# Kernel optimization log

Hardware: AMD Instinct MI355X
Metric: run time of the kernel (lower is better)

Reference implementation:

```python
import jax, jax.numpy as jnp
import numpy as np

H = 8          # num_attention_heads
E = 768        # hidden_size
D = E // H     # attention_head_size = 96
LN_EPS = 1e-5


def setup_inputs() -> dict:
    key = jax.random.key(0)
    ks = jax.random.split(key, 12)
    B, S = 2, 2048
    inp = {
        "hidden_states": jax.random.normal(ks[0], (B, S, E), jnp.float32),
        "distance_matrix": jax.random.uniform(ks[1], (B, S, S), jnp.float32),
        "angle_matrix": jax.random.uniform(ks[2], (B, S, S), jnp.float32),
        "attention_mask": jnp.ones((B, S), jnp.float32),
        # Linear params, stored [in, out] so y = x @ W + b
        "Wq": jax.random.normal(ks[3], (E, E), jnp.float32) * 0.02,
        "bq": jnp.zeros((E,), jnp.float32),
        "Wk": jax.random.normal(ks[4], (E, E), jnp.float32) * 0.02,
        "bk": jnp.zeros((E,), jnp.float32),
        "Wv": jax.random.normal(ks[5], (E, E), jnp.float32) * 0.02,
        "bv": jnp.zeros((E,), jnp.float32),
        # distance_embedding / angle_embedding: Linear(1,1) -> scalar w,b
        "dist_w": jax.random.normal(ks[6], (), jnp.float32) * 0.5,
        "dist_b": jnp.zeros((), jnp.float32),
        "ang_w": jax.random.normal(ks[7], (), jnp.float32) * 0.5,
        "ang_b": jnp.zeros((), jnp.float32),
        "Wo": jax.random.normal(ks[8], (E, E), jnp.float32) * 0.02,
        "bo": jnp.zeros((E,), jnp.float32),
        "ln_gamma": jnp.ones((E,), jnp.float32),
        "ln_beta": jnp.zeros((E,), jnp.float32),
    }
    return inp


def _attention(hidden_states, distance_matrix, angle_matrix, attention_mask,
               Wq, bq, Wk, bk, Wv, bv, dist_w, dist_b, ang_w, ang_b,
               Wo, bo, ln_gamma, ln_beta):
    B, S, _ = hidden_states.shape
    # project and split heads -> [B, H, S, D]
    def heads(x):
        return x.reshape(B, S, H, D).transpose(0, 2, 1, 3)
    q = heads(hidden_states @ Wq + bq)
    k = heads(hidden_states @ Wk + bk)
    v = heads(hidden_states @ Wv + bv)

    scores = jnp.einsum("bhqd,bhkd->bhqk", q, k) / jnp.sqrt(jnp.float32(D))
    # fused pairwise biases, broadcast over heads
    bias = (dist_w * distance_matrix + dist_b) + (ang_w * angle_matrix + ang_b)
    scores = scores + bias[:, None, :, :]
    # additive mask: mask is [B, S] over key dim
    scores = scores + ((1.0 - attention_mask) * -10000.0)[:, None, None, :]

    probs = jax.nn.softmax(scores, axis=-1)  # dropout is identity at eval
    ctx = jnp.einsum("bhqk,bhkd->bhqd", probs, v)
    ctx = ctx.transpose(0, 2, 1, 3).reshape(B, S, E)

    out = ctx @ Wo + bo  # output dropout identity at eval
    res = out + hidden_states
    mu = jnp.mean(res, axis=-1, keepdims=True)
    var = jnp.var(res, axis=-1, keepdims=True)
    out = (res - mu) * jax.lax.rsqrt(var + LN_EPS) * ln_gamma + ln_beta
    return out, probs


def reference(hidden_states, distance_matrix, angle_matrix, attention_mask,
              Wq, bq, Wk, bk, Wv, bv, dist_w, dist_b, ang_w, ang_b,
              Wo, bo, ln_gamma, ln_beta):
    return _attention(hidden_states, distance_matrix, angle_matrix, attention_mask,
                      Wq, bq, Wk, bk, Wv, bv, dist_w, dist_b, ang_w, ang_b,
                      Wo, bo, ln_gamma, ln_beta)
```

## Files before the change

### kernel.cpp

```cpp
#include <hip/hip_runtime.h>
#include <math.h>

#define S_LEN 2048
#define BATCH 2
#define EMB 768
#define NH 8
#define HD 96
#define NTOK (BATCH*S_LEN)
#define RSQRT_D 0.10206207261596575f

typedef unsigned short u16;
typedef __attribute__((ext_vector_type(8))) short bf16x8;
typedef __attribute__((ext_vector_type(4))) float f32x4;

#define MFMA16(a,b,c) __builtin_amdgcn_mfma_f32_16x16x32_bf16(a,b,c,0,0,0)

__device__ __forceinline__ u16 f2bf(float f){
    unsigned u = __float_as_uint(f);
    return (u16)((u + 0x7fffu + ((u>>16)&1u)) >> 16);
}
__device__ __forceinline__ float bf2f(unsigned u){
    return __uint_as_float(u << 16);
}

union U16x8 { u16 u[8]; float4 f4; };
union U16x4 { u16 u[4]; uint2 v2; };

__global__ __launch_bounds__(256) void cvt_bf16_kernel(
    const float* __restrict__ src, u16* __restrict__ dst, int n4)
{
    int i = blockIdx.x * 256 + threadIdx.x;
    if (i < n4) {
        float4 v = ((const float4*)src)[i];
        U16x4 o;
        o.u[0] = f2bf(v.x); o.u[1] = f2bf(v.y); o.u[2] = f2bf(v.z); o.u[3] = f2bf(v.w);
        *(uint2*)(dst + (size_t)i*4) = o.v2;
    }
}

__global__ __launch_bounds__(256) void transcvt_kernel(
    const float* __restrict__ W, u16* __restrict__ Wt)
{
    __shared__ float T[64][65];
    const int t = threadIdx.x;
    const int k0 = blockIdx.y * 64, n0 = blockIdx.x * 64;
    #pragma unroll
    for (int i = 0; i < 4; ++i) {
        int idx = t + 256*i;
        int r = idx >> 4, c4 = idx & 15;
        float4 v = *(const float4*)(W + (size_t)(k0 + r)*EMB + n0 + c4*4);
        T[r][c4*4+0] = v.x; T[r][c4*4+1] = v.y; T[r][c4*4+2] = v.z; T[r][c4*4+3] = v.w;
    }
    __syncthreads();
    #pragma unroll
    for (int i = 0; i < 2; ++i) {
        int idx = t + 256*i;
        int n = idx >> 3, c = idx & 7;
        U16x8 o;
        #pragma unroll
        for (int e = 0; e < 8; ++e) o.u[e] = f2bf(T[c*8+e][n]);
        *(float4*)(Wt + (size_t)(n0 + n)*EMB + k0 + c*8) = o.f4;
    }
}

__global__ __launch_bounds__(256) void qkv_mfma_kernel(
    const u16* __restrict__ hsb,
    const u16* __restrict__ WqT, const float* __restrict__ bq,
    const u16* __restrict__ WkT, const float* __restrict__ bk,
    const u16* __restrict__ WvT, const float* __restrict__ bv,
    u16* __restrict__ qo, u16* __restrict__ ko, u16* __restrict__ vo)
{
    const u16* Wt; const float* bias; u16* out;
    if (blockIdx.z == 0)      { Wt = WqT; bias = bq; out = qo; }
    else if (blockIdx.z == 1) { Wt = WkT; bias = bk; out = ko; }
    else                      { Wt = WvT; bias = bv; out = vo; }

    __shared__ __align__(16) u16 As[64*64];
    __shared__ __align__(16) u16 Bs[64*64];
    const int tid = threadIdx.x;
    const int w = tid >> 6, lane = tid & 63, lh = lane & 15, g = lane >> 4;
    const int wm = w >> 1, wn = w & 1;
    const int row0 = blockIdx.y * 64, col0 = blockIdx.x * 64;

    f32x4 acc[2][2];
    #pragma unroll
    for (int i = 0; i < 2; ++i)
        #pragma unroll
        for (int j = 0; j < 2; ++j) acc[i][j] = (f32x4){0.f,0.f,0.f,0.f};

    for (int k0 = 0; k0 < EMB; k0 += 64) {
        __syncthreads();
        #pragma unroll
        for (int i = 0; i < 2; ++i) {
            int idx = tid + 256*i;
            int r = idx >> 3, c = idx & 7;
            float4 a4 = *(const float4*)(hsb + (size_t)(row0 + r)*EMB + k0 + c*8);
            *(float4*)(As + ((size_t)r*8 + (c ^ (r & 7)))*8) = a4;
            float4 b4 = *(const float4*)(Wt + (size_t)(col0 + r)*EMB + k0 + c*8);
            *(float4*)(Bs + ((size_t)r*8 + (c ^ (r & 7)))*8) = b4;
        }
        __syncthreads();
        bf16x8 af[2][2], bfr[2][2];
        #pragma unroll
        for (int mt = 0; mt < 2; ++mt)
            #pragma unroll
            for (int kk = 0; kk < 2; ++kk) {
                int r = wm*32 + mt*16 + lh;
                af[mt][kk] = *(const bf16x8*)(As + ((size_t)r*8 + ((kk*4+g) ^ (lh & 7)))*8);
            }
        #pragma unroll
        for (int nt = 0; nt < 2; ++nt)
            #pragma unroll
            for (int kk = 0; kk < 2; ++kk) {
                int r = wn*32 + nt*16 + lh;
                bfr[nt][kk] = *(const bf16x8*)(Bs + ((size_t)r*8 + ((kk*4+g) ^ (lh & 7)))*8);
            }
        #pragma unroll
        for (int mt = 0; mt < 2; ++mt)
            #pragma unroll
            for (int nt = 0; nt < 2; ++nt)
                #pragma unroll
                for (int kk = 0; kk < 2; ++kk)
                    acc[mt][nt] = MFMA16(af[mt][kk], bfr[nt][kk], acc[mt][nt]);
    }

    #pragma unroll
    for (int mt = 0; mt < 2; ++mt)
        #pragma unroll
        for (int nt = 0; nt < 2; ++nt)
            #pragma unroll
            for (int r = 0; r < 4; ++r) {
                int tt = row0 + wm*32 + mt*16 + g*4 + r;
                int o  = col0 + wn*32 + nt*16 + lh;
                float val = acc[mt][nt][r] + bias[o];
                int b = tt >> 11, s = tt & (S_LEN - 1);
                int h = o / HD, d = o - h*HD;
                out[((size_t)(b*NH + h)*S_LEN + s)*HD + d] = f2bf(val);
            }
}

__global__ __launch_bounds__(256) void vtrans_kernel(
    const u16* __restrict__ vb, u16* __restrict__ vt)
{
    const int bh = blockIdx.y;
    const int s0 = blockIdx.x * 64;
    __shared__ __align__(16) u16 T[64*96];
    const int t = threadIdx.x;
    #pragma unroll
    for (int i = 0; i < 3; ++i) {
        int idx = t + 256*i;
        int s = idx / 12, c = idx % 12;
        float4 v = *(const float4*)(vb + ((size_t)bh*S_LEN + s0 + s)*HD + c*8);
        *(float4*)(T + ((size_t)s*12 + c)*8) = v;
    }
    __syncthreads();
    #pragma unroll
    for (int i = 0; i < 3; ++i) {
        int idx = t + 256*i;
        int d = idx >> 3, c = idx & 7;
        U16x8 o;
        #pragma unroll
        for (int e = 0; e < 8; ++e) o.u[e] = T[(size_t)(c*8+e)*HD + d];
        *(float4*)(vt + ((size_t)bh*HD + d)*S_LEN + s0 + c*8) = o.f4;
    }
}

__global__ __launch_bounds__(512) void fused_attn_kernel(
    const u16* __restrict__ qbf, const u16* __restrict__ kbf,
    const u16* __restrict__ vt,
    const float* __restrict__ dist, const float* __restrict__ ang,
    const float* __restrict__ mask,
    const float* __restrict__ pdw, const float* __restrict__ pdb,
    const float* __restrict__ paw, const float* __restrict__ pab,
    float* __restrict__ probs, u16* __restrict__ ctxb)
{
    const int bh = blockIdx.y, b = bh >> 3, h = bh & 7;
    const int q0 = blockIdx.x * 32;
    const int tid = threadIdx.x;
    const int lane = tid & 63, w = tid >> 6, lh = lane & 15, g = lane >> 4;
    const int rt = w >> 2;
    const int ct = w & 3;

    __shared__ __align__(16) u16 Us[32*2048];
    __shared__ __align__(16) u16 Ks[64*96];
    __shared__ __align__(16) float Sf[32*68];
    __shared__ float mL[32];

    const int kr_s = tid / 12, kc_s = tid - (tid / 12) * 12;
    const int kr2_s = (tid + 512) / 12, kc2_s = (tid + 512) - ((tid + 512) / 12) * 12;
    const int vr_s = tid >> 3, vc_s = tid & 7;
    const int vr2_s = (tid + 512) >> 3, vc2_s = (tid + 512) & 7;

    u16* Qtmp = (u16*)Sf;
    if (tid < 384) {
        int r = tid / 12, c = tid % 12;
        float4 v = *(const float4*)(qbf + ((size_t)bh*S_LEN + q0 + r)*HD + c*8);
        *(float4*)(Qtmp + ((size_t)r*12 + (c ^ ((r >> 1) & 3)))*8) = v;
    }
    {
        float4 v = *(const float4*)(kbf + ((size_t)bh*S_LEN + kr_s)*HD + kc_s*8);
        *(float4*)(Ks + ((size_t)kr_s*12 + (kc_s ^ ((kr_s >> 1) & 3)))*8) = v;
        if (tid < 256) {
            float4 v2 = *(const float4*)(kbf + ((size_t)bh*S_LEN + kr2_s)*HD + kc2_s*8);
            *(float4*)(Ks + ((size_t)kr2_s*12 + (kc2_s ^ ((kr2_s >> 1) & 3)))*8) = v2;
        }
    }
    __syncthreads();
    bf16x8 qf[3];
    #pragma unroll
    for (int kk = 0; kk < 3; ++kk) {
        int r = rt*16 + lh;
        qf[kk] = *(const bf16x8*)(Qtmp + ((size_t)r*12 + ((kk*4+g) ^ ((r >> 1) & 3)))*8);
    }
    __syncthreads();

    const float DW = *pdw, AW = *paw, CB = *pdb + *pab;
    const int trow = tid >> 4;
    const int c4   = tid & 15;
    const size_t drow = ((size_t)b*S_LEN + q0 + trow)*S_LEN;
    const int uoff = (trow*8 + ((c4 >> 1) ^ (trow & 7)))*8 + (c4 & 1)*4;

    float lpart = 0.f;

    for (int kt = 0; kt < 32; ++kt) {
        int coff = kt*64 + c4*4;
        float4 kreg0, kreg1;
        if (kt < 31) {
            kreg0 = *(const float4*)(kbf + ((size_t)bh*S_LEN + (kt+1)*64 + kr_s)*HD + kc_s*8);
            if (tid < 256)
                kreg1 = *(const float4*)(kbf + ((size_t)bh*S_LEN + (kt+1)*64 + kr2_s)*HD + kc2_s*8);
        }
        float4 d4 = *(const float4*)(dist + drow + coff);
        float4 g4 = *(const float4*)(ang  + drow + coff);
        float4 m4 = *(const float4*)(mask + b*S_LEN + coff);

        __builtin_amdgcn_s_setprio(1);
        f32x4 acc = (f32x4){0.f,0.f,0.f,0.f};
        #pragma unroll
        for (int kk = 0; kk < 3; ++kk) {
            int kr = ct*16 + lh;
            bf16x8 kf = *(const bf16x8*)(Ks + ((size_t)kr*12 + ((kk*4+g) ^ ((kr >> 1) & 3)))*8);
            acc = MFMA16(qf[kk], kf, acc);
        }
        __builtin_amdgcn_s_setprio(0);
        #pragma unroll
        for (int r = 0; r < 4; ++r)
            Sf[(rt*16 + g*4 + r)*68 + ct*16 + lh] = acc[r];
        __syncthreads();

        float4 s4 = *(const float4*)&Sf[trow*68 + c4*4];
        float e0 = __expf(s4.x*RSQRT_D + DW*d4.x + AW*g4.x + CB + (1.f - m4.x) * -10000.f);
        float e1 = __expf(s4.y*RSQRT_D + DW*d4.y + AW*g4.y + CB + (1.f - m4.y) * -10000.f);
        float e2 = __expf(s4.z*RSQRT_D + DW*d4.z + AW*g4.z + CB + (1.f - m4.z) * -10000.f);
        float e3 = __expf(s4.w*RSQRT_D + DW*d4.w + AW*g4.w + CB + (1.f - m4.w) * -10000.f);
        lpart += (e0 + e1) + (e2 + e3);
        U16x4 uk;
        uk.u[0] = f2bf(e0); uk.u[1] = f2bf(e1); uk.u[2] = f2bf(e2); uk.u[3] = f2bf(e3);
        *(uint2*)(Us + (size_t)kt*2048 + uoff) = uk.v2;

        if (kt < 31) {
            *(float4*)(Ks + ((size_t)kr_s*12 + (kc_s ^ ((kr_s >> 1) & 3)))*8) = kreg0;
            if (tid < 256)
                *(float4*)(Ks + ((size_t)kr2_s*12 + (kc2_s ^ ((kr2_s >> 1) & 3)))*8) = kreg1;
        }
        __syncthreads();
    }

    #pragma unroll
    for (int off = 1; off <= 8; off <<= 1) lpart += __shfl_xor(lpart, off);
    if (c4 == 0) mL[trow] = 1.0f / lpart;
    {
        float4 v4 = *(const float4*)(vt + ((size_t)bh*HD + vr_s)*S_LEN + vc_s*8);
        *(float4*)(Ks + ((size_t)vr_s*8 + (vc_s ^ (vr_s & 7)))*8) = v4;
        if (tid < 256) {
            float4 v42 = *(const float4*)(vt + ((size_t)bh*HD + vr2_s)*S_LEN + vc2_s*8);
            *(float4*)(Ks + ((size_t)vr2_s*8 + (vc2_s ^ (vr2_s & 7)))*8) = v42;
        }
    }
    __syncthreads();

    const float invl_row = mL[trow];
    const int dt1 = ct;
    const bool two = (ct < 2);
    const int dt2 = ct + 4;
    f32x4 accA = (f32x4){0.f,0.f,0.f,0.f};
    f32x4 accB = (f32x4){0.f,0.f,0.f,0.f};

    for (int kt = 0; kt < 32; ++kt) {
        float4 vreg0, vreg1;
        if (kt < 31) {
            vreg0 = *(const float4*)(vt + ((size_t)bh*HD + vr_s)*S_LEN + (kt+1)*64 + vc_s*8);
            if (tid < 256)
                vreg1 = *(const float4*)(vt + ((size_t)bh*HD + vr2_s)*S_LEN + (kt+1)*64 + vc2_s*8);
        }
        {
            uint2 uu = *(const uint2*)(Us + (size_t)kt*2048 + uoff);
            float4 p;
            p.x = bf2f(uu.x & 0xffffu)*invl_row; p.y = bf2f(uu.x >> 16)*invl_row;
            p.z = bf2f(uu.y & 0xffffu)*invl_row; p.w = bf2f(uu.y >> 16)*invl_row;
            *(float4*)(probs + ((size_t)bh*S_LEN + q0 + trow)*S_LEN + kt*64 + c4*4) = p;
        }
        int prow = rt*16 + lh;
        bf16x8 pa[2];
        #pragma unroll
        for (int kk = 0; kk < 2; ++kk)
            pa[kk] = *(const bf16x8*)(Us + (size_t)kt*2048 + ((size_t)prow*8 + ((kk*4+g) ^ (prow & 7)))*8);
        __builtin_amdgcn_s_setprio(1);
        #pragma unroll
        for (int kk = 0; kk < 2; ++kk) {
            int vr = dt1*16 + lh;
            bf16x8 vf = *(const bf16x8*)(Ks + ((size_t)vr*8 + ((kk*4+g) ^ (vr & 7)))*8);
            accA = MFMA16(pa[kk], vf, accA);
        }
        if (two) {
            #pragma unroll
            for (int kk = 0; kk < 2; ++kk) {
                int vr = dt2*16 + lh;
                bf16x8 vf = *(const bf16x8*)(Ks + ((size_t)vr*8 + ((kk*4+g) ^ (vr & 7)))*8);
                accB = MFMA16(pa[kk], vf, accB);
            }
        }
        __builtin_amdgcn_s_setprio(0);
        __syncthreads();
        if (kt < 31) {
            *(float4*)(Ks + ((size_t)vr_s*8 + (vc_s ^ (vr_s & 7)))*8) = vreg0;
            if (tid < 256)
                *(float4*)(Ks + ((size_t)vr2_s*8 + (vc2_s ^ (vr2_s & 7)))*8) = vreg1;
        }
        __syncthreads();
    }

    float ils[4];
    #pragma unroll
    for (int r = 0; r < 4; ++r) ils[r] = mL[rt*16 + g*4 + r];
    #pragma unroll
    for (int r = 0; r < 4; ++r) {
        int qrow = q0 + rt*16 + g*4 + r;
        ctxb[((size_t)(b*S_LEN + qrow))*EMB + h*HD + dt1*16 + lh] = f2bf(accA[r] * ils[r]);
        if (two)
            ctxb[((size_t)(b*S_LEN + qrow))*EMB + h*HD + dt2*16 + lh] = f2bf(accB[r] * ils[r]);
    }
}

__global__ __launch_bounds__(256) void out_mfma_kernel(
    const u16* __restrict__ ctxb, const u16* __restrict__ WoT,
    const float* __restrict__ bo, const float* __restrict__ hs,
    float* __restrict__ res)
{
    __shared__ __align__(16) u16 As[64*64];
    __shared__ __align__(16) u16 Bs[64*64];
    const int tid = threadIdx.x;
    const int w = tid >> 6, lane = tid & 63, lh = lane & 15, g = lane >> 4;
    const int wm = w >> 1, wn = w & 1;
    const int row0 = blockIdx.y * 64, col0 = blockIdx.x * 64;

    f32x4 acc[2][2];
    #pragma unroll
    for (int i = 0; i < 2; ++i)
        #pragma unroll
        for (int j = 0; j < 2; ++j) acc[i][j] = (f32x4){0.f,0.f,0.f,0.f};

    for (int k0 = 0; k0 < EMB; k0 += 64) {
        __syncthreads();
        #pragma unroll
        for (int i = 0; i < 2; ++i) {
            int idx = tid + 256*i;
            int r = idx >> 3, c = idx & 7;
            float4 a4 = *(const float4*)(ctxb + (size_t)(row0 + r)*EMB + k0 + c*8);
            *(float4*)(As + ((size_t)r*8 + (c ^ (r & 7)))*8) = a4;
            float4 b4 = *(const float4*)(WoT + (size_t)(col0 + r)*EMB + k0 + c*8);
            *(float4*)(Bs + ((size_t)r*8 + (c ^ (r & 7)))*8) = b4;
        }
        __syncthreads();
        bf16x8 af[2][2], bfr[2][2];
        #pragma unroll
        for (int mt = 0; mt < 2; ++mt)
            #pragma unroll
            for (int kk = 0; kk < 2; ++kk) {
                int r = wm*32 + mt*16 + lh;
                af[mt][kk] = *(const bf16x8*)(As + ((size_t)r*8 + ((kk*4+g) ^ (lh & 7)))*8);
            }
        #pragma unroll
        for (int nt = 0; nt < 2; ++nt)
            #pragma unroll
            for (int kk = 0; kk < 2; ++kk) {
                int r = wn*32 + nt*16 + lh;
                bfr[nt][kk] = *(const bf16x8*)(Bs + ((size_t)r*8 + ((kk*4+g) ^ (lh & 7)))*8);
            }
        #pragma unroll
        for (int mt = 0; mt < 2; ++mt)
            #pragma unroll
            for (int nt = 0; nt < 2; ++nt)
                #pragma unroll
                for (int kk = 0; kk < 2; ++kk)
                    acc[mt][nt] = MFMA16(af[mt][kk], bfr[nt][kk], acc[mt][nt]);
    }

    #pragma unroll
    for (int mt = 0; mt < 2; ++mt)
        #pragma unroll
        for (int nt = 0; nt < 2; ++nt)
            #pragma unroll
            for (int r = 0; r < 4; ++r) {
                int tt = row0 + wm*32 + mt*16 + g*4 + r;
                int o  = col0 + wn*32 + nt*16 + lh;
                res[(size_t)tt*EMB + o] = acc[mt][nt][r] + bo[o] + hs[(size_t)tt*EMB + o];
            }
}

__device__ __forceinline__ float block_sum256(float v, float* red) {
    #pragma unroll
    for (int off = 32; off > 0; off >>= 1) v += __shfl_down(v, off);
    int lane = threadIdx.x & 63, w = threadIdx.x >> 6;
    __syncthreads();
    if (lane == 0) red[w] = v;
    __syncthreads();
    return red[0] + red[1] + red[2] + red[3];
}

__global__ __launch_bounds__(256) void ln_kernel(
    float* __restrict__ res, const float* __restrict__ gamma, const float* __restrict__ beta)
{
    const int t = blockIdx.x;
    float* row = res + (size_t)t * EMB;
    const int tid = threadIdx.x;
    __shared__ float red[4];

    float x0 = row[tid], x1 = row[tid + 256], x2 = row[tid + 512];
    float s = block_sum256(x0 + x1 + x2, red);
    float mu = s * (1.0f / (float)EMB);
    float d0 = x0 - mu, d1 = x1 - mu, d2 = x2 - mu;
    float sq = block_sum256(d0*d0 + d1*d1 + d2*d2, red);
    float var = sq * (1.0f / (float)EMB);
    float scale = rsqrtf(var + 1e-5f);

    row[tid]       = d0 * scale * gamma[tid]       + beta[tid];
    row[tid + 256] = d1 * scale * gamma[tid + 256] + beta[tid + 256];
    row[tid + 512] = d2 * scale * gamma[tid + 512] + beta[tid + 512];
}

extern "C" void kernel_launch(void* const* d_in, const int* in_sizes, int n_in,
                              void* d_out, int out_size, void* d_ws, size_t ws_size,
                              hipStream_t stream)
{
    (void)in_sizes; (void)n_in; (void)out_size; (void)ws_size;

    const float* hs   = (const float*)d_in[0];
    const float* dist = (const float*)d_in[1];
    const float* ang  = (const float*)d_in[2];
    const float* mask = (const float*)d_in[3];
    const float* Wq = (const float*)d_in[4];  const float* bq = (const float*)d_in[5];
    const float* Wk = (const float*)d_in[6];  const float* bk = (const float*)d_in[7];
    const float* Wv = (const float*)d_in[8];  const float* bv = (const float*)d_in[9];
    const float* dw = (const float*)d_in[10]; const float* db = (const float*)d_in[11];
    const float* aw = (const float*)d_in[12]; const float* ab = (const float*)d_in[13];
    const float* Wo = (const float*)d_in[14]; const float* bo = (const float*)d_in[15];
    const float* gamma = (const float*)d_in[16]; const float* beta = (const float*)d_in[17];

    float* out   = (float*)d_out;
    float* probs = out + (size_t)NTOK * EMB;

    u16* hsb = (u16*)d_ws;
    u16* WqT = hsb + (size_t)NTOK*EMB;
    u16* WkT = WqT + (size_t)EMB*EMB;
    u16* WvT = WkT + (size_t)EMB*EMB;
    u16* WoT = WvT + (size_t)EMB*EMB;
    u16* qb  = WoT + (size_t)EMB*EMB;
    u16* kb  = qb + (size_t)NTOK*EMB;
    u16* vb  = kb + (size_t)NTOK*EMB;
    u16* vtb = vb + (size_t)NTOK*EMB;
    u16* ctxb = qb;

    cvt_bf16_kernel<<<dim3(NTOK*EMB/4/256), dim3(256), 0, stream>>>(hs, hsb, NTOK*EMB/4);
    transcvt_kernel<<<dim3(12,12), dim3(256), 0, stream>>>(Wq, WqT);
    transcvt_kernel<<<dim3(12,12), dim3(256), 0, stream>>>(Wk, WkT);
    transcvt_kernel<<<dim3(12,12), dim3(256), 0, stream>>>(Wv, WvT);
    transcvt_kernel<<<dim3(12,12), dim3(256), 0, stream>>>(Wo, WoT);

    qkv_mfma_kernel<<<dim3(EMB/64, NTOK/64, 3), dim3(256), 0, stream>>>(
        hsb, WqT, bq, WkT, bk, WvT, bv, qb, kb, vb);

    vtrans_kernel<<<dim3(S_LEN/64, BATCH*NH), dim3(256), 0, stream>>>(vb, vtb);

    fused_attn_kernel<<<dim3(S_LEN/32, BATCH*NH), dim3(512), 0, stream>>>(
        qb, kb, vtb, dist, ang, mask, dw, db, aw, ab, probs, ctxb);

    out_mfma_kernel<<<dim3(EMB/64, NTOK/64), dim3(256), 0, stream>>>(
        ctxb, WoT, bo, hs, out);

    ln_kernel<<<dim3(NTOK), dim3(256), 0, stream>>>(out, gamma, beta);
}
```

Baseline: 260.1 us.

## Deepen K/V and bias prefetch to two tiles ahead in attention loops

Unrolls the QK-softmax and PV loops by two and keeps two register sets of K/V tile loads in flight, issued two tiles ahead of use. The distance, angle and mask loads are also issued one tile early, so global-memory latency is better hidden behind the MFMA and exp work. In the QK loop the K shared-memory store now happens right after the MFMA sync instead of after the epilogue. This costs extra registers, which may reduce occupancy.

```diff
diff --git a/kernel.cpp b/kernel.cpp
--- a/kernel.cpp
+++ b/kernel.cpp
@@ -191,6 +191,12 @@
     const int vr_s = tid >> 3, vc_s = tid & 7;
     const int vr2_s = (tid + 512) >> 3, vc2_s = (tid + 512) & 7;
 
+    const float DW = *pdw, AW = *paw, CB = *pdb + *pab;
+    const int trow = tid >> 4;
+    const int c4   = tid & 15;
+    const size_t drow = ((size_t)b*S_LEN + q0 + trow)*S_LEN;
+    const int uoff = (trow*8 + ((c4 >> 1) ^ (trow & 7)))*8 + (c4 & 1)*4;
+
     u16* Qtmp = (u16*)Sf;
     if (tid < 384) {
         int r = tid / 12, c = tid % 12;
@@ -205,6 +211,17 @@
             *(float4*)(Ks + ((size_t)kr2_s*12 + (kc2_s ^ ((kr2_s >> 1) & 3)))*8) = v2;
         }
     }
+    float4 kA0, kA1, kB0, kB1;
+    kA0 = *(const float4*)(kbf + ((size_t)bh*S_LEN + 1*64 + kr_s)*HD + kc_s*8);
+    if (tid < 256)
+        kA1 = *(const float4*)(kbf + ((size_t)bh*S_LEN + 1*64 + kr2_s)*HD + kc2_s*8);
+    kB0 = *(const float4*)(kbf + ((size_t)bh*S_LEN + 2*64 + kr_s)*HD + kc_s*8);
+    if (tid < 256)
+        kB1 = *(const float4*)(kbf + ((size_t)bh*S_LEN + 2*64 + kr2_s)*HD + kc2_s*8);
+    float4 dc4 = *(const float4*)(dist + drow + c4*4);
+    float4 gc4 = *(const float4*)(ang  + drow + c4*4);
+    float4 mc4 = *(const float4*)(mask + b*S_LEN + c4*4);
+
     __syncthreads();
     bf16x8 qf[3];
     #pragma unroll
@@ -214,26 +231,10 @@
     }
     __syncthreads();
 
-    const float DW = *pdw, AW = *paw, CB = *pdb + *pab;
-    const int trow = tid >> 4;
-    const int c4   = tid & 15;
-    const size_t drow = ((size_t)b*S_LEN + q0 + trow)*S_LEN;
-    const int uoff = (trow*8 + ((c4 >> 1) ^ (trow & 7)))*8 + (c4 & 1)*4;
-
     float lpart = 0.f;
-
-    for (int kt = 0; kt < 32; ++kt) {
-        int coff = kt*64 + c4*4;
-        float4 kreg0, kreg1;
-        if (kt < 31) {
-            kreg0 = *(const float4*)(kbf + ((size_t)bh*S_LEN + (kt+1)*64 + kr_s)*HD + kc_s*8);
-            if (tid < 256)
-                kreg1 = *(const float4*)(kbf + ((size_t)bh*S_LEN + (kt+1)*64 + kr2_s)*HD + kc2_s*8);
-        }
-        float4 d4 = *(const float4*)(dist + drow + coff);
-        float4 g4 = *(const float4*)(ang  + drow + coff);
-        float4 m4 = *(const float4*)(mask + b*S_LEN + coff);
-
+    float4 dN4, gN4, mN4;
+
+    auto qkmfma = [&]() {
         __builtin_amdgcn_s_setprio(1);
         f32x4 acc = (f32x4){0.f,0.f,0.f,0.f};
         #pragma unroll
@@ -246,8 +247,8 @@
         #pragma unroll
         for (int r = 0; r < 4; ++r)
             Sf[(rt*16 + g*4 + r)*68 + ct*16 + lh] = acc[r];
-        __syncthreads();
-
+    };
+    auto epiA = [&](int kt, const float4& d4, const float4& g4, const float4& m4) {
         float4 s4 = *(const float4*)&Sf[trow*68 + c4*4];
         float e0 = __expf(s4.x*RSQRT_D + DW*d4.x + AW*g4.x + CB + (1.f - m4.x) * -10000.f);
         float e1 = __expf(s4.y*RSQRT_D + DW*d4.y + AW*g4.y + CB + (1.f - m4.y) * -10000.f);
@@ -257,12 +258,49 @@
         U16x4 uk;
         uk.u[0] = f2bf(e0); uk.u[1] = f2bf(e1); uk.u[2] = f2bf(e2); uk.u[3] = f2bf(e3);
         *(uint2*)(Us + (size_t)kt*2048 + uoff) = uk.v2;
-
-        if (kt < 31) {
-            *(float4*)(Ks + ((size_t)kr_s*12 + (kc_s ^ ((kr_s >> 1) & 3)))*8) = kreg0;
-            if (tid < 256)
-                *(float4*)(Ks + ((size_t)kr2_s*12 + (kc2_s ^ ((kr2_s >> 1) & 3)))*8) = kreg1;
-        }
+    };
+
+    for (int kt = 0; kt < 32; kt += 2) {
+        qkmfma();
+        __syncthreads();
+        {
+            *(float4*)(Ks + ((size_t)kr_s*12 + (kc_s ^ ((kr_s >> 1) & 3)))*8) = kA0;
+            if (tid < 256)
+                *(float4*)(Ks + ((size_t)kr2_s*12 + (kc2_s ^ ((kr2_s >> 1) & 3)))*8) = kA1;
+        }
+        {
+            int coff = (kt+1)*64 + c4*4;
+            dN4 = *(const float4*)(dist + drow + coff);
+            gN4 = *(const float4*)(ang  + drow + coff);
+            mN4 = *(const float4*)(mask + b*S_LEN + coff);
+        }
+        if (kt + 3 < 32) {
+            kA0 = *(const float4*)(kbf + ((size_t)bh*S_LEN + (kt+3)*64 + kr_s)*HD + kc_s*8);
+            if (tid < 256)
+                kA1 = *(const float4*)(kbf + ((size_t)bh*S_LEN + (kt+3)*64 + kr2_s)*HD + kc2_s*8);
+        }
+        epiA(kt, dc4, gc4, mc4);
+        __syncthreads();
+
+        qkmfma();
+        __syncthreads();
+        if (kt + 2 < 32) {
+            *(float4*)(Ks + ((size_t)kr_s*12 + (kc_s ^ ((kr_s >> 1) & 3)))*8) = kB0;
+            if (tid < 256)
+                *(float4*)(Ks + ((size_t)kr2_s*12 + (kc2_s ^ ((kr2_s >> 1) & 3)))*8) = kB1;
+        }
+        if (kt + 2 < 32) {
+            int coff = (kt+2)*64 + c4*4;
+            dc4 = *(const float4*)(dist + drow + coff);
+            gc4 = *(const float4*)(ang  + drow + coff);
+            mc4 = *(const float4*)(mask + b*S_LEN + coff);
+        }
+        if (kt + 4 < 32) {
+            kB0 = *(const float4*)(kbf + ((size_t)bh*S_LEN + (kt+4)*64 + kr_s)*HD + kc_s*8);
+            if (tid < 256)
+                kB1 = *(const float4*)(kbf + ((size_t)bh*S_LEN + (kt+4)*64 + kr2_s)*HD + kc2_s*8);
+        }
+        epiA(kt+1, dN4, gN4, mN4);
         __syncthreads();
     }
 
@@ -277,6 +315,13 @@
             *(float4*)(Ks + ((size_t)vr2_s*8 + (vc2_s ^ (vr2_s & 7)))*8) = v42;
         }
     }
+    float4 vA0, vA1, vB0, vB1;
+    vA0 = *(const float4*)(vt + ((size_t)bh*HD + vr_s)*S_LEN + 1*64 + vc_s*8);
+    if (tid < 256)
+        vA1 = *(const float4*)(vt + ((size_t)bh*HD + vr2_s)*S_LEN + 1*64 + vc2_s*8);
+    vB0 = *(const float4*)(vt + ((size_t)bh*HD + vr_s)*S_LEN + 2*64 + vc_s*8);
+    if (tid < 256)
+        vB1 = *(const float4*)(vt + ((size_t)bh*HD + vr2_s)*S_LEN + 2*64 + vc2_s*8);
     __syncthreads();
 
     const float invl_row = mL[trow];
@@ -286,20 +331,12 @@
     f32x4 accA = (f32x4){0.f,0.f,0.f,0.f};
     f32x4 accB = (f32x4){0.f,0.f,0.f,0.f};
 
-    for (int kt = 0; kt < 32; ++kt) {
-        float4 vreg0, vreg1;
-        if (kt < 31) {
-            vreg0 = *(const float4*)(vt + ((size_t)bh*HD + vr_s)*S_LEN + (kt+1)*64 + vc_s*8);
-            if (tid < 256)
-                vreg1 = *(const float4*)(vt + ((size_t)bh*HD + vr2_s)*S_LEN + (kt+1)*64 + vc2_s*8);
-        }
-        {
-            uint2 uu = *(const uint2*)(Us + (size_t)kt*2048 + uoff);
-            float4 p;
-            p.x = bf2f(uu.x & 0xffffu)*invl_row; p.y = bf2f(uu.x >> 16)*invl_row;
-            p.z = bf2f(uu.y & 0xffffu)*invl_row; p.w = bf2f(uu.y >> 16)*invl_row;
-            *(float4*)(probs + ((size_t)bh*S_LEN + q0 + trow)*S_LEN + kt*64 + c4*4) = p;
-        }
+    auto pvstep = [&](int kt) {
+        uint2 uu = *(const uint2*)(Us + (size_t)kt*2048 + uoff);
+        float4 p;
+        p.x = bf2f(uu.x & 0xffffu)*invl_row; p.y = bf2f(uu.x >> 16)*invl_row;
+        p.z = bf2f(uu.y & 0xffffu)*invl_row; p.w = bf2f(uu.y >> 16)*invl_row;
+        *(float4*)(probs + ((size_t)bh*S_LEN + q0 + trow)*S_LEN + kt*64 + c4*4) = p;
         int prow = rt*16 + lh;
         bf16x8 pa[2];
         #pragma unroll
@@ -321,11 +358,34 @@
             }
         }
         __builtin_amdgcn_s_setprio(0);
-        __syncthreads();
-        if (kt < 31) {
-            *(float4*)(Ks + ((size_t)vr_s*8 + (vc_s ^ (vr_s & 7)))*8) = vreg0;
-            if (tid < 256)
-                *(float4*)(Ks + ((size_t)vr2_s*8 + (vc2_s ^ (vr2_s & 7)))*8) = vreg1;
+    };
+
+    for (int kt = 0; kt < 32; kt += 2) {
+        pvstep(kt);
+        __syncthreads();
+        {
+            *(float4*)(Ks + ((size_t)vr_s*8 + (vc_s ^ (vr_s & 7)))*8) = vA0;
+            if (tid < 256)
+                *(float4*)(Ks + ((size_t)vr2_s*8 + (vc2_s ^ (vr2_s & 7)))*8) = vA1;
+        }
+        if (kt + 3 < 32) {
+            vA0 = *(const float4*)(vt + ((size_t)bh*HD + vr_s)*S_LEN + (kt+3)*64 + vc_s*8);
+            if (tid < 256)
+                vA1 = *(const float4*)(vt + ((size_t)bh*HD + vr2_s)*S_LEN + (kt+3)*64 + vc2_s*8);
+        }
+        __syncthreads();
+
+        pvstep(kt+1);
+        __syncthreads();
+        if (kt + 2 < 32) {
+            *(float4*)(Ks + ((size_t)vr_s*8 + (vc_s ^ (vr_s & 7)))*8) = vB0;
+            if (tid < 256)
+                *(float4*)(Ks + ((size_t)vr2_s*8 + (vc2_s ^ (vr2_s & 7)))*8) = vB1;
+        }
+        if (kt + 4 < 32) {
+            vB0 = *(const float4*)(vt + ((size_t)bh*HD + vr_s)*S_LEN + (kt+4)*64 + vc_s*8);
+            if (tid < 256)
+                vB1 = *(const float4*)(vt + ((size_t)bh*HD + vr2_s)*S_LEN + (kt+4)*64 + vc2_s*8);
         }
         __syncthreads();
     }
```

Measured after the change: 264.1 us. No clear change (+1.6%).

## Split fused attention into row-sum pass and recompute-plus-PV pass

Applied to the files above, without the earlier changes.

Replaces the single fused attention kernel, which cached all exponentiated scores for a 32-row tile in 128KB of LDS, with two kernels. The first computes QK^T plus biases and writes only the per-row exp sums. The second recomputes the scores, normalizes and writes probs, then does PV through a small 64-column P buffer. This cuts LDS use per block to raise occupancy, but it doubles the QK^T work and the reads of the distance and angle matrices.

```diff
diff --git a/kernel.cpp b/kernel.cpp
--- a/kernel.cpp
+++ b/kernel.cpp
@@ -165,31 +165,26 @@
     }
 }
 
-__global__ __launch_bounds__(512) void fused_attn_kernel(
+__global__ __launch_bounds__(512) void scores_l_kernel(
     const u16* __restrict__ qbf, const u16* __restrict__ kbf,
-    const u16* __restrict__ vt,
     const float* __restrict__ dist, const float* __restrict__ ang,
     const float* __restrict__ mask,
     const float* __restrict__ pdw, const float* __restrict__ pdb,
     const float* __restrict__ paw, const float* __restrict__ pab,
-    float* __restrict__ probs, u16* __restrict__ ctxb)
-{
-    const int bh = blockIdx.y, b = bh >> 3, h = bh & 7;
+    float* __restrict__ lrow)
+{
+    const int bh = blockIdx.y, b = bh >> 3;
     const int q0 = blockIdx.x * 32;
     const int tid = threadIdx.x;
     const int lane = tid & 63, w = tid >> 6, lh = lane & 15, g = lane >> 4;
     const int rt = w >> 2;
     const int ct = w & 3;
 
-    __shared__ __align__(16) u16 Us[32*2048];
     __shared__ __align__(16) u16 Ks[64*96];
     __shared__ __align__(16) float Sf[32*68];
-    __shared__ float mL[32];
 
     const int kr_s = tid / 12, kc_s = tid - (tid / 12) * 12;
     const int kr2_s = (tid + 512) / 12, kc2_s = (tid + 512) - ((tid + 512) / 12) * 12;
-    const int vr_s = tid >> 3, vc_s = tid & 7;
-    const int vr2_s = (tid + 512) >> 3, vc2_s = (tid + 512) & 7;
 
     u16* Qtmp = (u16*)Sf;
     if (tid < 384) {
@@ -215,10 +210,8 @@
     __syncthreads();
 
     const float DW = *pdw, AW = *paw, CB = *pdb + *pab;
-    const int trow = tid >> 4;
-    const int c4   = tid & 15;
+    const int trow = tid >> 4, c4 = tid & 15;
     const size_t drow = ((size_t)b*S_LEN + q0 + trow)*S_LEN;
-    const int uoff = (trow*8 + ((c4 >> 1) ^ (trow & 7)))*8 + (c4 & 1)*4;
 
     float lpart = 0.f;
 
@@ -248,91 +241,176 @@
             Sf[(rt*16 + g*4 + r)*68 + ct*16 + lh] = acc[r];
         __syncthreads();
 
+        if (kt < 31) {
+            *(float4*)(Ks + ((size_t)kr_s*12 + (kc_s ^ ((kr_s >> 1) & 3)))*8) = kreg0;
+            if (tid < 256)
+                *(float4*)(Ks + ((size_t)kr2_s*12 + (kc2_s ^ ((kr2_s >> 1) & 3)))*8) = kreg1;
+        }
         float4 s4 = *(const float4*)&Sf[trow*68 + c4*4];
         float e0 = __expf(s4.x*RSQRT_D + DW*d4.x + AW*g4.x + CB + (1.f - m4.x) * -10000.f);
         float e1 = __expf(s4.y*RSQRT_D + DW*d4.y + AW*g4.y + CB + (1.f - m4.y) * -10000.f);
         float e2 = __expf(s4.z*RSQRT_D + DW*d4.z + AW*g4.z + CB + (1.f - m4.z) * -10000.f);
         float e3 = __expf(s4.w*RSQRT_D + DW*d4.w + AW*g4.w + CB + (1.f - m4.w) * -10000.f);
         lpart += (e0 + e1) + (e2 + e3);
-        U16x4 uk;
-        uk.u[0] = f2bf(e0); uk.u[1] = f2bf(e1); uk.u[2] = f2bf(e2); uk.u[3] = f2bf(e3);
-        *(uint2*)(Us + (size_t)kt*2048 + uoff) = uk.v2;
-
-        if (kt < 31) {
-            *(float4*)(Ks + ((size_t)kr_s*12 + (kc_s ^ ((kr_s >> 1) & 3)))*8) = kreg0;
-            if (tid < 256)
-                *(float4*)(Ks + ((size_t)kr2_s*12 + (kc2_s ^ ((kr2_s >> 1) & 3)))*8) = kreg1;
-        }
         __syncthreads();
     }
 
     #pragma unroll
     for (int off = 1; off <= 8; off <<= 1) lpart += __shfl_xor(lpart, off);
-    if (c4 == 0) mL[trow] = 1.0f / lpart;
+    if (c4 == 0) lrow[(bh << 11) + q0 + trow] = lpart;
+}
+
+__global__ __launch_bounds__(512) void attn_pv_kernel(
+    const u16* __restrict__ qbf, const u16* __restrict__ kbf,
+    const u16* __restrict__ vt,
+    const float* __restrict__ dist, const float* __restrict__ ang,
+    const float* __restrict__ mask,
+    const float* __restrict__ pdw, const float* __restrict__ pdb,
+    const float* __restrict__ paw, const float* __restrict__ pab,
+    const float* __restrict__ lrow,
+    float* __restrict__ probs, u16* __restrict__ ctxb)
+{
+    const int bh = blockIdx.y, b = bh >> 3, h = bh & 7;
+    const int q0 = blockIdx.x * 32;
+    const int tid = threadIdx.x;
+    const int lane = tid & 63, w = tid >> 6, lh = lane & 15, g = lane >> 4;
+    const int rt = w >> 2;
+    const int ct = w & 3;
+
+    __shared__ __align__(16) u16 Ks[64*96];
+    __shared__ __align__(16) u16 Vs[96*64];
+    __shared__ __align__(16) float Sf[32*68];
+    __shared__ __align__(16) u16 Ps[32*64];
+
+    const int kr_s = tid / 12, kc_s = tid - (tid / 12) * 12;
+    const int kr2_s = (tid + 512) / 12, kc2_s = (tid + 512) - ((tid + 512) / 12) * 12;
+    const int vr_s = tid >> 3, vc_s = tid & 7;
+    const int vr2_s = (tid + 512) >> 3, vc2_s = (tid + 512) & 7;
+
+    u16* Qtmp = (u16*)Sf;
+    if (tid < 384) {
+        int r = tid / 12, c = tid % 12;
+        float4 v = *(const float4*)(qbf + ((size_t)bh*S_LEN + q0 + r)*HD + c*8);
+        *(float4*)(Qtmp + ((size_t)r*12 + (c ^ ((r >> 1) & 3)))*8) = v;
+    }
     {
+        float4 v = *(const float4*)(kbf + ((size_t)bh*S_LEN + kr_s)*HD + kc_s*8);
+        *(float4*)(Ks + ((size_t)kr_s*12 + (kc_s ^ ((kr_s >> 1) & 3)))*8) = v;
+        if (tid < 256) {
+            float4 v2 = *(const float4*)(kbf + ((size_t)bh*S_LEN + kr2_s)*HD + kc2_s*8);
+            *(float4*)(Ks + ((size_t)kr2_s*12 + (kc2_s ^ ((kr2_s >> 1) & 3)))*8) = v2;
+        }
         float4 v4 = *(const float4*)(vt + ((size_t)bh*HD + vr_s)*S_LEN + vc_s*8);
-        *(float4*)(Ks + ((size_t)vr_s*8 + (vc_s ^ (vr_s & 7)))*8) = v4;
+        *(float4*)(Vs + ((size_t)vr_s*8 + (vc_s ^ (vr_s & 7)))*8) = v4;
         if (tid < 256) {
             float4 v42 = *(const float4*)(vt + ((size_t)bh*HD + vr2_s)*S_LEN + vc2_s*8);
-            *(float4*)(Ks + ((size_t)vr2_s*8 + (vc2_s ^ (vr2_s & 7)))*8) = v42;
-        }
-    }
-    __syncthreads();
-
-    const float invl_row = mL[trow];
+            *(float4*)(Vs + ((size_t)vr2_s*8 + (vc2_s ^ (vr2_s & 7)))*8) = v42;
+        }
+    }
+    __syncthreads();
+    bf16x8 qf[3];
+    #pragma unroll
+    for (int kk = 0; kk < 3; ++kk) {
+        int r = rt*16 + lh;
+        qf[kk] = *(const bf16x8*)(Qtmp + ((size_t)r*12 + ((kk*4+g) ^ ((r >> 1) & 3)))*8);
+    }
+    __syncthreads();
+
+    const float DW = *pdw, AW = *paw, CB = *pdb + *pab;
+    const int trow = tid >> 4, c4 = tid & 15;
+    const size_t drow = ((size_t)b*S_LEN + q0 + trow)*S_LEN;
+    const int uoffP = (trow*8 + ((c4 >> 1) ^ (trow & 7)))*8 + (c4 & 1)*4;
+    const float invl_row = 1.0f / lrow[(bh << 11) + q0 + trow];
+
     const int dt1 = ct;
     const bool two = (ct < 2);
     const int dt2 = ct + 4;
+    const int prowPV = rt*16 + lh;
     f32x4 accA = (f32x4){0.f,0.f,0.f,0.f};
     f32x4 accB = (f32x4){0.f,0.f,0.f,0.f};
 
     for (int kt = 0; kt < 32; ++kt) {
-        float4 vreg0, vreg1;
+        int coff = kt*64 + c4*4;
+        float4 kp0, kp1, vp0, vp1;
         if (kt < 31) {
-            vreg0 = *(const float4*)(vt + ((size_t)bh*HD + vr_s)*S_LEN + (kt+1)*64 + vc_s*8);
+            kp0 = *(const float4*)(kbf + ((size_t)bh*S_LEN + (kt+1)*64 + kr_s)*HD + kc_s*8);
             if (tid < 256)
-                vreg1 = *(const float4*)(vt + ((size_t)bh*HD + vr2_s)*S_LEN + (kt+1)*64 + vc2_s*8);
+                kp1 = *(const float4*)(kbf + ((size_t)bh*S_LEN + (kt+1)*64 + kr2_s)*HD + kc2_s*8);
+            vp0 = *(const float4*)(vt + ((size_t)bh*HD + vr_s)*S_LEN + (kt+1)*64 + vc_s*8);
+            if (tid < 256)
+                vp1 = *(const float4*)(vt + ((size_t)bh*HD + vr2_s)*S_LEN + (kt+1)*64 + vc2_s*8);
+        }
+        float4 d4 = *(const float4*)(dist + drow + coff);
+        float4 g4 = *(const float4*)(ang  + drow + coff);
+        float4 m4 = *(const float4*)(mask + b*S_LEN + coff);
+
+        __builtin_amdgcn_s_setprio(1);
+        f32x4 acc = (f32x4){0.f,0.f,0.f,0.f};
+        #pragma unroll
+        for (int kk = 0; kk < 3; ++kk) {
+            int kr = ct*16 + lh;
+            bf16x8 kf = *(const bf16x8*)(Ks + ((size_t)kr*12 + ((kk*4+g) ^ ((kr >> 1) & 3)))*8);
+            acc = MFMA16(qf[kk], kf, acc);
+        }
+        __builtin_amdgcn_s_setprio(0);
+        #pragma unroll
+        for (int r = 0; r < 4; ++r)
+            Sf[(rt*16 + g*4 + r)*68 + ct*16 + lh] = acc[r];
+        __syncthreads();
+
+        if (kt < 31) {
+            *(float4*)(Ks + ((size_t)kr_s*12 + (kc_s ^ ((kr_s >> 1) & 3)))*8) = kp0;
+            if (tid < 256)
+                *(float4*)(Ks + ((size_t)kr2_s*12 + (kc2_s ^ ((kr2_s >> 1) & 3)))*8) = kp1;
         }
         {
-            uint2 uu = *(const uint2*)(Us + (size_t)kt*2048 + uoff);
+            float4 s4 = *(const float4*)&Sf[trow*68 + c4*4];
+            float e0 = __expf(s4.x*RSQRT_D + DW*d4.x + AW*g4.x + CB + (1.f - m4.x) * -10000.f);
+            float e1 = __expf(s4.y*RSQRT_D + DW*d4.y + AW*g4.y + CB + (1.f - m4.y) * -10000.f);
+            float e2 = __expf(s4.z*RSQRT_D + DW*d4.z + AW*g4.z + CB + (1.f - m4.z) * -10000.f);
+            float e3 = __expf(s4.w*RSQRT_D + DW*d4.w + AW*g4.w + CB + (1.f - m4.w) * -10000.f);
             float4 p;
-            p.x = bf2f(uu.x & 0xffffu)*invl_row; p.y = bf2f(uu.x >> 16)*invl_row;
-            p.z = bf2f(uu.y & 0xffffu)*invl_row; p.w = bf2f(uu.y >> 16)*invl_row;
-            *(float4*)(probs + ((size_t)bh*S_LEN + q0 + trow)*S_LEN + kt*64 + c4*4) = p;
-        }
-        int prow = rt*16 + lh;
+            p.x = e0*invl_row; p.y = e1*invl_row; p.z = e2*invl_row; p.w = e3*invl_row;
+            *(float4*)(probs + ((size_t)bh*S_LEN + q0 + trow)*S_LEN + coff) = p;
+            U16x4 uk;
+            uk.u[0] = f2bf(e0); uk.u[1] = f2bf(e1); uk.u[2] = f2bf(e2); uk.u[3] = f2bf(e3);
+            *(uint2*)(Ps + uoffP) = uk.v2;
+        }
+        __syncthreads();
+
         bf16x8 pa[2];
         #pragma unroll
         for (int kk = 0; kk < 2; ++kk)
-            pa[kk] = *(const bf16x8*)(Us + (size_t)kt*2048 + ((size_t)prow*8 + ((kk*4+g) ^ (prow & 7)))*8);
+            pa[kk] = *(const bf16x8*)(Ps + ((size_t)prowPV*8 + ((kk*4+g) ^ (prowPV & 7)))*8);
         __builtin_amdgcn_s_setprio(1);
         #pragma unroll
         for (int kk = 0; kk < 2; ++kk) {
             int vr = dt1*16 + lh;
-            bf16x8 vf = *(const bf16x8*)(Ks + ((size_t)vr*8 + ((kk*4+g) ^ (vr & 7)))*8);
+            bf16x8 vf = *(const bf16x8*)(Vs + ((size_t)vr*8 + ((kk*4+g) ^ (vr & 7)))*8);
             accA = MFMA16(pa[kk], vf, accA);
         }
         if (two) {
             #pragma unroll
             for (int kk = 0; kk < 2; ++kk) {
                 int vr = dt2*16 + lh;
-                bf16x8 vf = *(const bf16x8*)(Ks + ((size_t)vr*8 + ((kk*4+g) ^ (vr & 7)))*8);
+                bf16x8 vf = *(const bf16x8*)(Vs + ((size_t)vr*8 + ((kk*4+g) ^ (vr & 7)))*8);
                 accB = MFMA16(pa[kk], vf, accB);
             }
         }
         __builtin_amdgcn_s_setprio(0);
         __syncthreads();
+
         if (kt < 31) {
-            *(float4*)(Ks + ((size_t)vr_s*8 + (vc_s ^ (vr_s & 7)))*8) = vreg0;
+            *(float4*)(Vs + ((size_t)vr_s*8 + (vc_s ^ (vr_s & 7)))*8) = vp0;
             if (tid < 256)
-                *(float4*)(Ks + ((size_t)vr2_s*8 + (vc2_s ^ (vr2_s & 7)))*8) = vreg1;
-        }
-        __syncthreads();
+                *(float4*)(Vs + ((size_t)vr2_s*8 + (vc2_s ^ (vr2_s & 7)))*8) = vp1;
+        }
     }
 
     float ils[4];
     #pragma unroll
-    for (int r = 0; r < 4; ++r) ils[r] = mL[rt*16 + g*4 + r];
+    for (int r = 0; r < 4; ++r)
+        ils[r] = 1.0f / lrow[(bh << 11) + q0 + rt*16 + g*4 + r];
     #pragma unroll
     for (int r = 0; r < 4; ++r) {
         int qrow = q0 + rt*16 + g*4 + r;
@@ -470,6 +548,7 @@
     u16* vb  = kb + (size_t)NTOK*EMB;
     u16* vtb = vb + (size_t)NTOK*EMB;
     u16* ctxb = qb;
+    float* lrow = (float*)(vtb + (size_t)NTOK*EMB);
 
     cvt_bf16_kernel<<<dim3(NTOK*EMB/4/256), dim3(256), 0, stream>>>(hs, hsb, NTOK*EMB/4);
     transcvt_kernel<<<dim3(12,12), dim3(256), 0, stream>>>(Wq, WqT);
@@ -482,8 +561,11 @@
 
     vtrans_kernel<<<dim3(S_LEN/64, BATCH*NH), dim3(256), 0, stream>>>(vb, vtb);
 
-    fused_attn_kernel<<<dim3(S_LEN/32, BATCH*NH), dim3(512), 0, stream>>>(
-        qb, kb, vtb, dist, ang, mask, dw, db, aw, ab, probs, ctxb);
+    scores_l_kernel<<<dim3(S_LEN/32, BATCH*NH), dim3(512), 0, stream>>>(
+        qb, kb, dist, ang, mask, dw, db, aw, ab, lrow);
+
+    attn_pv_kernel<<<dim3(S_LEN/32, BATCH*NH), dim3(512), 0, stream>>>(
+        qb, kb, vtb, dist, ang, mask, dw, db, aw, ab, lrow, probs, ctxb);
 
     out_mfma_kernel<<<dim3(EMB/64, NTOK/64), dim3(256), 0, stream>>>(
         ctxb, WoT, bo, hs, out);
```

After: 240.2 us (median of 2 runs). 7.7% less time.
